# Kernel optimization log

Hardware: AMD Instinct MI355X
Metric: run time of the kernel (lower is better)

## Reference

```python
import jax, jax.numpy as jnp
import numpy as np

NUM_HEADS = 16
HEAD_DIM = 64  # 1024 / 16


def setup_inputs() -> dict:
    key = jax.random.key(0)
    ks = jax.random.split(key, 8)
    B, S, D = 2, 2048, 1024
    s = 0.02
    return {
        "hidden_states_q": jax.random.normal(ks[0], (B, S, D), jnp.float32),
        "hidden_states_k": jax.random.normal(ks[1], (B, S, D), jnp.float32),
        "hidden_states_v": jax.random.normal(ks[2], (B, S, D), jnp.float32),
        "Wq": jax.random.normal(ks[3], (D, D), jnp.float32) * s,
        "bq": jnp.zeros((D,), jnp.float32),
        "Wk": jax.random.normal(ks[4], (D, D), jnp.float32) * s,
        "bk": jnp.zeros((D,), jnp.float32),
        "Wv": jax.random.normal(ks[5], (D, D), jnp.float32) * s,
        "bv": jnp.zeros((D,), jnp.float32),
        "Wp": jax.random.normal(ks[6], (D, D), jnp.float32) * s,
        "bp": jnp.zeros((D,), jnp.float32),
    }


def _split_heads(x):
    B, S, D = x.shape
    return x.reshape(B, S, NUM_HEADS, HEAD_DIM).transpose(0, 2, 1, 3)  # [B,H,S,dh]


def reference(hidden_states_q, hidden_states_k, hidden_states_v,
              Wq, bq, Wk, bk, Wv, bv, Wp, bp):
    # Projections (Linear / Conv1D are both x @ W + b in this parameterization)
    q = _split_heads(hidden_states_q @ Wq + bq)
    k = _split_heads(hidden_states_k @ Wk + bk)
    v = _split_heads(hidden_states_v @ Wv + bv)
    scale = 1.0 / jnp.sqrt(jnp.asarray(HEAD_DIM, q.dtype))
    # NOTE: no causal mask is applied in the original _attn (mask asserted None)
    attn = jnp.einsum("bhqd,bhkd->bhqk", q, k) * scale
    attn = jax.nn.softmax(attn, axis=-1)  # attn_dropout is identity in eval
    out = jnp.einsum("bhqk,bhkd->bhqd", attn, v)
    B, H, S, dh = out.shape
    out = out.transpose(0, 2, 1, 3).reshape(B, S, H * dh)
    out = out @ Wp + bp  # resid_dropout identity in eval
    return out
```

## Files before the change

### kernel.cpp

```cpp
#include <hip/hip_runtime.h>
#include <stdint.h>


typedef _Float16 f16;
typedef __attribute__((ext_vector_type(8))) _Float16 f16x8;
typedef __attribute__((ext_vector_type(4))) _Float16 f16x4;
typedef __attribute__((ext_vector_type(4))) float f32x4;
typedef __attribute__((ext_vector_type(16))) float f32x16;
typedef __attribute__((ext_vector_type(2))) unsigned u32x2;

#define NB 2
#define SEQ 2048
#define DMODEL 1024
#define NH 16
#define DH 64

#define QSCALE 0.1803368801111601f

__device__ __forceinline__ void gload_lds16(const void* g, void* l) {
  __builtin_amdgcn_global_load_lds(
      (const __attribute__((address_space(1))) unsigned int*)g,
      (__attribute__((address_space(3))) unsigned int*)l, 16, 0, 0);
}

__device__ __forceinline__ void plswap(unsigned& a, unsigned& b) {
  u32x2 r = __builtin_amdgcn_permlane32_swap(a, b, false, false);
  a = r[0];
  b = r[1];
}

__global__ __launch_bounds__(256) void cast_f16_3(
    const float* __restrict__ s0, const float* __restrict__ s1,
    const float* __restrict__ s2, f16* __restrict__ d0, f16* __restrict__ d1,
    f16* __restrict__ d2) {
  const float* src = blockIdx.z == 0 ? s0 : (blockIdx.z == 1 ? s1 : s2);
  f16* dst = blockIdx.z == 0 ? d0 : (blockIdx.z == 1 ? d1 : d2);
  int i = (blockIdx.x * 256 + threadIdx.x) * 8;
  float4 a = *(const float4*)(src + i);
  float4 b = *(const float4*)(src + i + 4);
  f16x8 o;
  o[0] = (f16)a.x; o[1] = (f16)a.y; o[2] = (f16)a.z; o[3] = (f16)a.w;
  o[4] = (f16)b.x; o[5] = (f16)b.y; o[6] = (f16)b.z; o[7] = (f16)b.w;
  *(f16x8*)(dst + i) = o;
}

__global__ __launch_bounds__(256) void transw(
    const float* __restrict__ w0, const float* __restrict__ w1,
    const float* __restrict__ w2, const float* __restrict__ w3,
    f16* __restrict__ t0, f16* __restrict__ t1, f16* __restrict__ t2,
    f16* __restrict__ t3) {
  __shared__ float tile[64][65];
  const float* W; f16* T;
  switch (blockIdx.z) {
    case 0: W = w0; T = t0; break;
    case 1: W = w1; T = t1; break;
    case 2: W = w2; T = t2; break;
    default: W = w3; T = t3; break;
  }
  int r0 = blockIdx.y * 64, c0 = blockIdx.x * 64;
  for (int it = 0; it < 16; ++it) {
    int idx = it * 256 + threadIdx.x;
    int r = idx >> 6, c = idx & 63;
    tile[r][c] = W[(size_t)(r0 + r) * DMODEL + c0 + c];
  }
  __syncthreads();
  for (int it = 0; it < 16; ++it) {
    int idx = it * 256 + threadIdx.x;
    int r = idx >> 6, c = idx & 63;
    T[(size_t)(c0 + r) * DMODEL + r0 + c] = (f16)tile[c][r];
  }
}

__global__ __launch_bounds__(256) void gemm128(
    const f16* __restrict__ xq, const f16* __restrict__ xk,
    const f16* __restrict__ xv, const f16* __restrict__ ao,
    const f16* __restrict__ wqt, const f16* __restrict__ wkt,
    const f16* __restrict__ wvt, const f16* __restrict__ wpt,
    const float* __restrict__ bq, const float* __restrict__ bk,
    const float* __restrict__ bv, const float* __restrict__ bp,
    f16* __restrict__ qo, f16* __restrict__ ko, f16* __restrict__ vto,
    float* __restrict__ out, int mode_base) {
  __shared__ char lds[32768];
  char* ldsA = lds;
  char* ldsB = lds + 16384;

  int mode = mode_base + blockIdx.z;
  const f16* Am; const f16* Bt; const float* bias; float oscale = 1.0f;
  if (mode == 0)      { Am = xq; Bt = wqt; bias = bq; oscale = QSCALE; }
  else if (mode == 1) { Am = xk; Bt = wkt; bias = bk; }
  else if (mode == 2) { Am = xv; Bt = wvt; bias = bv; }
  else                { Am = ao; Bt = wpt; bias = bp; }

  const int tid = threadIdx.x;
  const int l = tid & 63, w = tid >> 6;
  const int g = l >> 4, c = l & 15;
  const int wr = w >> 1, wc = w & 1;
  const int m0 = blockIdx.y * 128, n0 = blockIdx.x * 128;

  const int srow = w * 8 + (l >> 3);
  const int schunk = (l & 7) ^ ((l >> 3) & 7);

  f32x4 acc[4][4] = {};

  for (int k0 = 0; k0 < DMODEL; k0 += 64) {
#pragma unroll
    for (int it = 0; it < 4; ++it) {
      int row = it * 32 + srow;
      gload_lds16(Am + (size_t)(m0 + row) * DMODEL + k0 + schunk * 8,
                  ldsA + it * 4096 + w * 1024);
    }
#pragma unroll
    for (int it = 0; it < 4; ++it) {
      int row = it * 32 + srow;
      gload_lds16(Bt + (size_t)(n0 + row) * DMODEL + k0 + schunk * 8,
                  ldsB + it * 4096 + w * 1024);
    }
    __syncthreads();
    f16x8 af[2][4], bf[2][4];
#pragma unroll
    for (int kc = 0; kc < 2; ++kc)
#pragma unroll
      for (int i = 0; i < 4; ++i) {
        int row = wr * 64 + i * 16 + c;
        af[kc][i] = *(const f16x8*)(ldsA + row * 128 + (((kc * 4 + g) ^ (row & 7)) << 4));
        int rowb = wc * 64 + i * 16 + c;
        bf[kc][i] = *(const f16x8*)(ldsB + rowb * 128 + (((kc * 4 + g) ^ (rowb & 7)) << 4));
      }
#pragma unroll
    for (int kc = 0; kc < 2; ++kc)
#pragma unroll
      for (int i = 0; i < 4; ++i)
#pragma unroll
        for (int j = 0; j < 4; ++j)
          acc[i][j] = __builtin_amdgcn_mfma_f32_16x16x32_f16(af[kc][i], bf[kc][j],
                                                             acc[i][j], 0, 0, 0);
    __syncthreads();
  }

#pragma unroll
  for (int i = 0; i < 4; ++i) {
#pragma unroll
    for (int j = 0; j < 4; ++j) {
      int grb = m0 + wr * 64 + i * 16 + g * 4;
      int gc = n0 + wc * 64 + j * 16 + c;
      float bval = bias[gc];
      if (mode == 3) {
#pragma unroll
        for (int e = 0; e < 4; ++e)
          out[(size_t)(grb + e) * DMODEL + gc] = acc[i][j][e] + bval;
      } else if (mode == 2) {
        int b = grb >> 11, s = grb & 2047, h = gc >> 6, d = gc & 63;
        f16x4 pk;
#pragma unroll
        for (int e = 0; e < 4; ++e) pk[e] = (f16)(acc[i][j][e] + bval);
        *(f16x4*)(vto + ((size_t)((b * NH + h) * DH + d)) * SEQ + s) = pk;
      } else {
        f16* dst = (mode == 0) ? qo : ko;
        int b = grb >> 11, s = grb & 2047, h = gc >> 6, d = gc & 63;
#pragma unroll
        for (int e = 0; e < 4; ++e)
          dst[(((size_t)(b * NH + h) * SEQ) + (s + e)) * DH + d] =
              (f16)((acc[i][j][e] + bval) * oscale);
      }
    }
  }
}

__global__ __launch_bounds__(256, 2) void attn64(
    const f16* __restrict__ qg, const f16* __restrict__ kg,
    const f16* __restrict__ vtg, f16* __restrict__ aout) {
  __shared__ char lds[33792];

  const int tid = threadIdx.x;
  const int l = tid & 63, w = tid >> 6;
  const int q31 = l & 31;
  const bool hi = l >= 32;
  const int p = w & 1;
  const int qgrp = w >> 1;

  const int bid = blockIdx.x;
  const int bh = (bid & 7) + 8 * (bid >> 7);
  const int qc = (bid >> 3) & 15;
  const int q0 = qc * 128 + qgrp * 64;

  f16x8 qf0[4], qf1[4];
#pragma unroll
  for (int ks = 0; ks < 4; ++ks) {
    qf0[ks] = *(const f16x8*)(qg + ((size_t)bh * SEQ + q0 + q31) * DH + ks * 16 +
                              (hi ? 8 : 0));
    qf1[ks] = *(const f16x8*)(qg + ((size_t)bh * SEQ + q0 + 32 + q31) * DH +
                              ks * 16 + (hi ? 8 : 0));
  }

  float lsum0 = 0.0f, lsum1 = 0.0f;
  f32x16 oacc00 = {}, oacc01 = {}, oacc10 = {}, oacc11 = {};

  const int srow = w * 8 + (l >> 3);
  const int schunk = (l & 7) ^ ((l >> 3) & 7);

  auto stage = [&](int buf, int t) {
    char* baseK = lds + buf * 16384;
    char* baseV = baseK + 8192;
#pragma unroll
    for (int it = 0; it < 2; ++it) {
      int row = it * 32 + srow;
      gload_lds16(kg + ((size_t)bh * SEQ + t * 64 + row) * DH + schunk * 8,
                  baseK + it * 4096 + w * 1024);
      gload_lds16(vtg + ((size_t)bh * DH + row) * SEQ + t * 64 + schunk * 8,
                  baseV + it * 4096 + w * 1024);
    }
  };

  auto softmax = [&](const f32x16& st, float& lsum, unsigned* dw) {
    float ps[16];
#pragma unroll
    for (int r = 0; r < 16; ++r) ps[r] = exp2f(st[r]);
    {
      float t0 = (ps[0] + ps[1]) + (ps[2] + ps[3]);
      float t1 = (ps[4] + ps[5]) + (ps[6] + ps[7]);
      float t2 = (ps[8] + ps[9]) + (ps[10] + ps[11]);
      float t3 = (ps[12] + ps[13]) + (ps[14] + ps[15]);
      lsum += (t0 + t1) + (t2 + t3);
    }
#pragma unroll
    for (int i = 0; i < 8; ++i)
      dw[i] = __builtin_bit_cast(
          unsigned, __builtin_amdgcn_cvt_pkrtz(ps[2 * i], ps[2 * i + 1]));
    plswap(dw[0], dw[2]);
    plswap(dw[1], dw[3]);
    plswap(dw[4], dw[6]);
    plswap(dw[5], dw[7]);
  };

  stage(0, 0);

  for (int t = 0; t < 32; ++t) {
    int cur = t & 1;
    if (t + 1 < 32) {
      stage(cur ^ 1, t + 1);
      asm volatile("s_waitcnt vmcnt(4)" ::: "memory");
    } else {
      asm volatile("s_waitcnt vmcnt(0)" ::: "memory");
    }
    __builtin_amdgcn_s_barrier();
    __builtin_amdgcn_sched_barrier(0);

    const char* ldsK = lds + cur * 16384;
    const char* ldsV = ldsK + 8192;

    f32x16 st0 = {}, st1 = {};
    __builtin_amdgcn_s_setprio(1);
#pragma unroll
    for (int ks = 0; ks < 4; ++ks) {
      int row = p * 32 + q31;
      int ch = ((ks * 2 + (hi ? 1 : 0)) ^ (q31 & 7)) << 4;
      f16x8 kf = *(const f16x8*)(ldsK + row * 128 + ch);
      st0 = __builtin_amdgcn_mfma_f32_32x32x16_f16(kf, qf0[ks], st0, 0, 0, 0);
      st1 = __builtin_amdgcn_mfma_f32_32x32x16_f16(kf, qf1[ks], st1, 0, 0, 0);
    }
    __builtin_amdgcn_s_setprio(0);

    unsigned dw0[8], dw1[8];
    softmax(st0, lsum0, dw0);
    softmax(st1, lsum1, dw1);

    __builtin_amdgcn_s_setprio(1);
#pragma unroll
    for (int ks2 = 0; ks2 < 2; ++ks2) {
      union { unsigned u[4]; f16x8 v; } pb0, pb1;
      pb0.u[0] = dw0[ks2 * 4 + 0]; pb0.u[1] = dw0[ks2 * 4 + 1];
      pb0.u[2] = dw0[ks2 * 4 + 2]; pb0.u[3] = dw0[ks2 * 4 + 3];
      pb1.u[0] = dw1[ks2 * 4 + 0]; pb1.u[1] = dw1[ks2 * 4 + 1];
      pb1.u[2] = dw1[ks2 * 4 + 2]; pb1.u[3] = dw1[ks2 * 4 + 3];
      {
        int vrow = q31;
        int ch = ((p * 4 + ks2 * 2 + (hi ? 1 : 0)) ^ (vrow & 7)) << 4;
        f16x8 vf = *(const f16x8*)(ldsV + vrow * 128 + ch);
        oacc00 = __builtin_amdgcn_mfma_f32_32x32x16_f16(vf, pb0.v, oacc00, 0, 0, 0);
        oacc10 = __builtin_amdgcn_mfma_f32_32x32x16_f16(vf, pb1.v, oacc10, 0, 0, 0);
      }
      {
        int vrow = 32 + q31;
        int ch = ((p * 4 + ks2 * 2 + (hi ? 1 : 0)) ^ (vrow & 7)) << 4;
        f16x8 vf = *(const f16x8*)(ldsV + vrow * 128 + ch);
        oacc01 = __builtin_amdgcn_mfma_f32_32x32x16_f16(vf, pb0.v, oacc01, 0, 0, 0);
        oacc11 = __builtin_amdgcn_mfma_f32_32x32x16_f16(vf, pb1.v, oacc11, 0, 0, 0);
      }
    }
    __builtin_amdgcn_s_setprio(0);
    __builtin_amdgcn_sched_barrier(0);
    __builtin_amdgcn_s_barrier();
  }

  __builtin_amdgcn_s_barrier();
  char* reg = lds + qgrp * 16896;
  if (p == 1) {
#pragma unroll
    for (int j = 0; j < 8; ++j) {
      f32x4 c0, c1;
#pragma unroll
      for (int e = 0; e < 4; ++e) {
        c0[e] = (j < 4) ? oacc00[j * 4 + e] : oacc01[(j - 4) * 4 + e];
        c1[e] = (j < 4) ? oacc10[j * 4 + e] : oacc11[(j - 4) * 4 + e];
      }
      *(f32x4*)(reg + j * 1024 + l * 16) = c0;
      *(f32x4*)(reg + 8192 + j * 1024 + l * 16) = c1;
    }
    *(float*)(reg + 16384 + l * 4) = lsum0;
    *(float*)(reg + 16640 + l * 4) = lsum1;
  }
  __syncthreads();
  if (p == 0) {
#pragma unroll
    for (int j = 0; j < 8; ++j) {
      f32x4 c0 = *(const f32x4*)(reg + j * 1024 + l * 16);
      f32x4 c1 = *(const f32x4*)(reg + 8192 + j * 1024 + l * 16);
#pragma unroll
      for (int e = 0; e < 4; ++e) {
        if (j < 4) { oacc00[j * 4 + e] += c0[e]; oacc10[j * 4 + e] += c1[e]; }
        else       { oacc01[(j - 4) * 4 + e] += c0[e]; oacc11[(j - 4) * 4 + e] += c1[e]; }
      }
    }
    float lt0 = lsum0 + *(const float*)(reg + 16384 + l * 4);
    float lt1 = lsum1 + *(const float*)(reg + 16640 + l * 4);
    lt0 += __shfl_xor(lt0, 32);
    lt1 += __shfl_xor(lt1, 32);
    float inv0 = 1.0f / lt0, inv1 = 1.0f / lt1;
    const int b = bh >> 4, h = bh & 15;
#pragma unroll
    for (int f = 0; f < 2; ++f) {
      float inv = f ? inv1 : inv0;
      int s = q0 + f * 32 + q31;
#pragma unroll
      for (int dt = 0; dt < 2; ++dt)
#pragma unroll
        for (int rg = 0; rg < 4; ++rg) {
          f16x4 pk;
#pragma unroll
          for (int j = 0; j < 4; ++j) {
            float v = f ? (dt ? oacc11[rg * 4 + j] : oacc10[rg * 4 + j])
                        : (dt ? oacc01[rg * 4 + j] : oacc00[rg * 4 + j]);
            pk[j] = (f16)(v * inv);
          }
          int d0 = dt * 32 + rg * 8 + (hi ? 4 : 0);
          *(f16x4*)(aout + ((size_t)(b * SEQ + s)) * DMODEL + h * DH + d0) = pk;
        }
    }
  }
}

extern "C" void kernel_launch(void* const* d_in, const int* in_sizes, int n_in,
                              void* d_out, int out_size, void* d_ws, size_t ws_size,
                              hipStream_t stream) {
  const float* hq = (const float*)d_in[0];
  const float* hk = (const float*)d_in[1];
  const float* hv = (const float*)d_in[2];
  const float* Wq = (const float*)d_in[3];
  const float* bq = (const float*)d_in[4];
  const float* Wk = (const float*)d_in[5];
  const float* bk = (const float*)d_in[6];
  const float* Wv = (const float*)d_in[7];
  const float* bv = (const float*)d_in[8];
  const float* Wp = (const float*)d_in[9];
  const float* bp = (const float*)d_in[10];
  float* out = (float*)d_out;

  f16* xq  = (f16*)d_ws;
  f16* xk  = xq + 4194304;
  f16* xv  = xk + 4194304;
  f16* wqt = xv + 4194304;
  f16* wkt = wqt + 1048576;
  f16* wvt = wkt + 1048576;
  f16* wpt = wvt + 1048576;
  f16* qb  = wpt + 1048576;
  f16* kb  = qb + 4194304;
  f16* vtb = kb + 4194304;
  f16* ao  = vtb + 4194304;

  cast_f16_3<<<dim3(2048, 1, 3), 256, 0, stream>>>(hq, hk, hv, xq, xk, xv);
  transw<<<dim3(16, 16, 4), 256, 0, stream>>>(Wq, Wk, Wv, Wp, wqt, wkt, wvt, wpt);
  gemm128<<<dim3(8, 32, 3), 256, 0, stream>>>(xq, xk, xv, ao, wqt, wkt, wvt, wpt,
                                              bq, bk, bv, bp, qb, kb, vtb, out, 0);
  attn64<<<dim3(512), 256, 0, stream>>>(qb, kb, vtb, ao);
  gemm128<<<dim3(8, 32, 1), 256, 0, stream>>>(xq, xk, xv, ao, wqt, wkt, wvt, wpt,
                                              bq, bk, bv, bp, qb, kb, vtb, out, 3);
}
```

Before: 153.3 us.

## Merge prep kernels, retile output GEMM, use fdot2 row sums, drop setprio

Folds the input cast and the weight transpose into one launch, removing a kernel launch and its tail. The output projection gets its own kernel with 128x64 tiles, doubling the block count (256 to 512) for better CU occupancy. In attention, the softmax row sum is now computed with fdot2 over the packed f16 probabilities instead of f32 adds, and the s_setprio hints around the MFMA blocks are removed. Summing the rounded f16 values slightly changes the normalisation precision.

```diff
diff --git a/kernel.cpp b/kernel.cpp
--- a/kernel.cpp
+++ b/kernel.cpp
@@ -5,6 +5,7 @@
 typedef _Float16 f16;
 typedef __attribute__((ext_vector_type(8))) _Float16 f16x8;
 typedef __attribute__((ext_vector_type(4))) _Float16 f16x4;
+typedef __attribute__((ext_vector_type(2))) _Float16 f16x2;
 typedef __attribute__((ext_vector_type(4))) float f32x4;
 typedef __attribute__((ext_vector_type(16))) float f32x16;
 typedef __attribute__((ext_vector_type(2))) unsigned u32x2;
@@ -29,35 +30,36 @@
   b = r[1];
 }
 
-__global__ __launch_bounds__(256) void cast_f16_3(
-    const float* __restrict__ s0, const float* __restrict__ s1,
-    const float* __restrict__ s2, f16* __restrict__ d0, f16* __restrict__ d1,
-    f16* __restrict__ d2) {
-  const float* src = blockIdx.z == 0 ? s0 : (blockIdx.z == 1 ? s1 : s2);
-  f16* dst = blockIdx.z == 0 ? d0 : (blockIdx.z == 1 ? d1 : d2);
-  int i = (blockIdx.x * 256 + threadIdx.x) * 8;
-  float4 a = *(const float4*)(src + i);
-  float4 b = *(const float4*)(src + i + 4);
-  f16x8 o;
-  o[0] = (f16)a.x; o[1] = (f16)a.y; o[2] = (f16)a.z; o[3] = (f16)a.w;
-  o[4] = (f16)b.x; o[5] = (f16)b.y; o[6] = (f16)b.z; o[7] = (f16)b.w;
-  *(f16x8*)(dst + i) = o;
-}
-
-__global__ __launch_bounds__(256) void transw(
-    const float* __restrict__ w0, const float* __restrict__ w1,
-    const float* __restrict__ w2, const float* __restrict__ w3,
-    f16* __restrict__ t0, f16* __restrict__ t1, f16* __restrict__ t2,
-    f16* __restrict__ t3) {
+__global__ __launch_bounds__(256) void prep(
+    const float* __restrict__ hq, const float* __restrict__ hk,
+    const float* __restrict__ hv, f16* __restrict__ xq, f16* __restrict__ xk,
+    f16* __restrict__ xv, const float* __restrict__ w0,
+    const float* __restrict__ w1, const float* __restrict__ w2,
+    const float* __restrict__ w3, f16* __restrict__ t0, f16* __restrict__ t1,
+    f16* __restrict__ t2, f16* __restrict__ t3) {
   __shared__ float tile[64][65];
+  const int z = blockIdx.z;
+  if (z < 3) {
+    const float* src = z == 0 ? hq : (z == 1 ? hk : hv);
+    f16* dst = z == 0 ? xq : (z == 1 ? xk : xv);
+    int i = (blockIdx.x * 256 + threadIdx.x) * 8;
+    float4 a = *(const float4*)(src + i);
+    float4 b = *(const float4*)(src + i + 4);
+    f16x8 o;
+    o[0] = (f16)a.x; o[1] = (f16)a.y; o[2] = (f16)a.z; o[3] = (f16)a.w;
+    o[4] = (f16)b.x; o[5] = (f16)b.y; o[6] = (f16)b.z; o[7] = (f16)b.w;
+    *(f16x8*)(dst + i) = o;
+    return;
+  }
+  if (blockIdx.x >= 256) return;
   const float* W; f16* T;
-  switch (blockIdx.z) {
+  switch (z - 3) {
     case 0: W = w0; T = t0; break;
     case 1: W = w1; T = t1; break;
     case 2: W = w2; T = t2; break;
     default: W = w3; T = t3; break;
   }
-  int r0 = blockIdx.y * 64, c0 = blockIdx.x * 64;
+  int r0 = (blockIdx.x >> 4) * 64, c0 = (blockIdx.x & 15) * 64;
   for (int it = 0; it < 16; ++it) {
     int idx = it * 256 + threadIdx.x;
     int r = idx >> 6, c = idx & 63;
@@ -73,23 +75,21 @@
 
 __global__ __launch_bounds__(256) void gemm128(
     const f16* __restrict__ xq, const f16* __restrict__ xk,
-    const f16* __restrict__ xv, const f16* __restrict__ ao,
+    const f16* __restrict__ xv,
     const f16* __restrict__ wqt, const f16* __restrict__ wkt,
-    const f16* __restrict__ wvt, const f16* __restrict__ wpt,
+    const f16* __restrict__ wvt,
     const float* __restrict__ bq, const float* __restrict__ bk,
-    const float* __restrict__ bv, const float* __restrict__ bp,
-    f16* __restrict__ qo, f16* __restrict__ ko, f16* __restrict__ vto,
-    float* __restrict__ out, int mode_base) {
+    const float* __restrict__ bv,
+    f16* __restrict__ qo, f16* __restrict__ ko, f16* __restrict__ vto) {
   __shared__ char lds[32768];
   char* ldsA = lds;
   char* ldsB = lds + 16384;
 
-  int mode = mode_base + blockIdx.z;
+  int mode = blockIdx.z;
   const f16* Am; const f16* Bt; const float* bias; float oscale = 1.0f;
   if (mode == 0)      { Am = xq; Bt = wqt; bias = bq; oscale = QSCALE; }
   else if (mode == 1) { Am = xk; Bt = wkt; bias = bk; }
-  else if (mode == 2) { Am = xv; Bt = wvt; bias = bv; }
-  else                { Am = ao; Bt = wpt; bias = bp; }
+  else                { Am = xv; Bt = wvt; bias = bv; }
 
   const int tid = threadIdx.x;
   const int l = tid & 63, w = tid >> 6;
@@ -144,11 +144,7 @@
       int grb = m0 + wr * 64 + i * 16 + g * 4;
       int gc = n0 + wc * 64 + j * 16 + c;
       float bval = bias[gc];
-      if (mode == 3) {
-#pragma unroll
-        for (int e = 0; e < 4; ++e)
-          out[(size_t)(grb + e) * DMODEL + gc] = acc[i][j][e] + bval;
-      } else if (mode == 2) {
+      if (mode == 2) {
         int b = grb >> 11, s = grb & 2047, h = gc >> 6, d = gc & 63;
         f16x4 pk;
 #pragma unroll
@@ -164,6 +160,76 @@
       }
     }
   }
+}
+
+__global__ __launch_bounds__(256) void gemm_out(
+    const f16* __restrict__ ao, const f16* __restrict__ wpt,
+    const float* __restrict__ bp, float* __restrict__ out) {
+  __shared__ char lds[24576];
+  char* ldsA = lds;
+  char* ldsB = lds + 16384;
+
+  const int tid = threadIdx.x;
+  const int l = tid & 63, w = tid >> 6;
+  const int g = l >> 4, c = l & 15;
+  const int wr = w >> 1, wc = w & 1;
+  const int m0 = blockIdx.y * 128, n0 = blockIdx.x * 64;
+
+  const int srow = w * 8 + (l >> 3);
+  const int schunk = (l & 7) ^ ((l >> 3) & 7);
+
+  f32x4 acc[4][2] = {};
+
+  for (int k0 = 0; k0 < DMODEL; k0 += 64) {
+#pragma unroll
+    for (int it = 0; it < 4; ++it) {
+      int row = it * 32 + srow;
+      gload_lds16(ao + (size_t)(m0 + row) * DMODEL + k0 + schunk * 8,
+                  ldsA + it * 4096 + w * 1024);
+    }
+#pragma unroll
+    for (int it = 0; it < 2; ++it) {
+      int row = it * 32 + srow;
+      gload_lds16(wpt + (size_t)(n0 + row) * DMODEL + k0 + schunk * 8,
+                  ldsB + it * 4096 + w * 1024);
+    }
+    __syncthreads();
+    f16x8 af[2][4], bf[2][2];
+#pragma unroll
+    for (int kc = 0; kc < 2; ++kc) {
+#pragma unroll
+      for (int i = 0; i < 4; ++i) {
+        int row = wr * 64 + i * 16 + c;
+        af[kc][i] = *(const f16x8*)(ldsA + row * 128 + (((kc * 4 + g) ^ (row & 7)) << 4));
+      }
+#pragma unroll
+      for (int j = 0; j < 2; ++j) {
+        int rowb = wc * 32 + j * 16 + c;
+        bf[kc][j] = *(const f16x8*)(ldsB + rowb * 128 + (((kc * 4 + g) ^ (rowb & 7)) << 4));
+      }
+    }
+#pragma unroll
+    for (int kc = 0; kc < 2; ++kc)
+#pragma unroll
+      for (int i = 0; i < 4; ++i)
+#pragma unroll
+        for (int j = 0; j < 2; ++j)
+          acc[i][j] = __builtin_amdgcn_mfma_f32_16x16x32_f16(af[kc][i], bf[kc][j],
+                                                             acc[i][j], 0, 0, 0);
+    __syncthreads();
+  }
+
+#pragma unroll
+  for (int i = 0; i < 4; ++i)
+#pragma unroll
+    for (int j = 0; j < 2; ++j) {
+      int grb = m0 + wr * 64 + i * 16 + g * 4;
+      int gc = n0 + wc * 32 + j * 16 + c;
+      float bval = bp[gc];
+#pragma unroll
+      for (int e = 0; e < 4; ++e)
+        out[(size_t)(grb + e) * DMODEL + gc] = acc[i][j][e] + bval;
+    }
 }
 
 __global__ __launch_bounds__(256, 2) void attn64(
@@ -211,21 +277,23 @@
     }
   };
 
+  const f16x2 one2 = {(f16)1.0f, (f16)1.0f};
+
   auto softmax = [&](const f32x16& st, float& lsum, unsigned* dw) {
     float ps[16];
 #pragma unroll
     for (int r = 0; r < 16; ++r) ps[r] = exp2f(st[r]);
-    {
-      float t0 = (ps[0] + ps[1]) + (ps[2] + ps[3]);
-      float t1 = (ps[4] + ps[5]) + (ps[6] + ps[7]);
-      float t2 = (ps[8] + ps[9]) + (ps[10] + ps[11]);
-      float t3 = (ps[12] + ps[13]) + (ps[14] + ps[15]);
-      lsum += (t0 + t1) + (t2 + t3);
-    }
 #pragma unroll
     for (int i = 0; i < 8; ++i)
       dw[i] = __builtin_bit_cast(
           unsigned, __builtin_amdgcn_cvt_pkrtz(ps[2 * i], ps[2 * i + 1]));
+    float sA = 0.0f, sB = 0.0f;
+#pragma unroll
+    for (int i = 0; i < 4; ++i) {
+      sA = __builtin_amdgcn_fdot2(__builtin_bit_cast(f16x2, dw[i]), one2, sA, false);
+      sB = __builtin_amdgcn_fdot2(__builtin_bit_cast(f16x2, dw[4 + i]), one2, sB, false);
+    }
+    lsum += sA + sB;
     plswap(dw[0], dw[2]);
     plswap(dw[1], dw[3]);
     plswap(dw[4], dw[6]);
@@ -249,7 +317,6 @@
     const char* ldsV = ldsK + 8192;
 
     f32x16 st0 = {}, st1 = {};
-    __builtin_amdgcn_s_setprio(1);
 #pragma unroll
     for (int ks = 0; ks < 4; ++ks) {
       int row = p * 32 + q31;
@@ -258,13 +325,11 @@
       st0 = __builtin_amdgcn_mfma_f32_32x32x16_f16(kf, qf0[ks], st0, 0, 0, 0);
       st1 = __builtin_amdgcn_mfma_f32_32x32x16_f16(kf, qf1[ks], st1, 0, 0, 0);
     }
-    __builtin_amdgcn_s_setprio(0);
 
     unsigned dw0[8], dw1[8];
     softmax(st0, lsum0, dw0);
     softmax(st1, lsum1, dw1);
 
-    __builtin_amdgcn_s_setprio(1);
 #pragma unroll
     for (int ks2 = 0; ks2 < 2; ++ks2) {
       union { unsigned u[4]; f16x8 v; } pb0, pb1;
@@ -287,7 +352,6 @@
         oacc11 = __builtin_amdgcn_mfma_f32_32x32x16_f16(vf, pb1.v, oacc11, 0, 0, 0);
       }
     }
-    __builtin_amdgcn_s_setprio(0);
     __builtin_amdgcn_sched_barrier(0);
     __builtin_amdgcn_s_barrier();
   }
@@ -377,11 +441,10 @@
   f16* vtb = kb + 4194304;
   f16* ao  = vtb + 4194304;
 
-  cast_f16_3<<<dim3(2048, 1, 3), 256, 0, stream>>>(hq, hk, hv, xq, xk, xv);
-  transw<<<dim3(16, 16, 4), 256, 0, stream>>>(Wq, Wk, Wv, Wp, wqt, wkt, wvt, wpt);
-  gemm128<<<dim3(8, 32, 3), 256, 0, stream>>>(xq, xk, xv, ao, wqt, wkt, wvt, wpt,
-                                              bq, bk, bv, bp, qb, kb, vtb, out, 0);
+  prep<<<dim3(2048, 1, 7), 256, 0, stream>>>(hq, hk, hv, xq, xk, xv,
+                                             Wq, Wk, Wv, Wp, wqt, wkt, wvt, wpt);
+  gemm128<<<dim3(8, 32, 3), 256, 0, stream>>>(xq, xk, xv, wqt, wkt, wvt,
+                                              bq, bk, bv, qb, kb, vtb);
   attn64<<<dim3(512), 256, 0, stream>>>(qb, kb, vtb, ao);
-  gemm128<<<dim3(8, 32, 1), 256, 0, stream>>>(xq, xk, xv, ao, wqt, wkt, wvt, wpt,
-                                              bq, bk, bv, bp, qb, kb, vtb, out, 3);
-}
+  gemm_out<<<dim3(16, 32), 256, 0, stream>>>(ao, wpt, bp, out);
+}
```

After: 142.7 us. 1.07x faster.
